# Optimization experiments

Measured on AMD Instinct MI355X. Metric: run time of the kernel, lower is better.

The kernel has to match this reference:

```python
import jax, jax.numpy as jnp
import numpy as np

TAU = 0.95
COEF = 0.5
LOG_CLAMP = -100.0  # torch BCELoss clamps log terms at -100


def setup_inputs() -> dict:
    key = jax.random.key(0)
    k1, k2, k3, k4, k5 = jax.random.split(key, 5)
    B, L = 4096, 2048
    eps = 1e-4
    # probabilities in (eps, 1-eps) so log / log1p are finite
    def prob(k, shape):
        return jax.random.uniform(k, shape, dtype=jnp.float32, minval=eps, maxval=1.0 - eps)
    truncation_output = prob(k1, (B, L, 1))
    view_1_output = prob(k2, (B, L, 1))
    view_2_output = prob(k3, (B, L, 1))
    view_3_output = prob(k4, (B, L, 1))
    labels = (jax.random.uniform(k5, (B, L)) < 0.1).astype(jnp.float32)
    return {
        "truncation_output": truncation_output,
        "view_1_output": view_1_output,
        "view_2_output": view_2_output,
        "view_3_output": view_3_output,
        "labels": labels,
    }


def _bce_div_batch(p, y):
    # nn.BCELoss() (mean reduction) then .div(batch_size)
    logp = jnp.maximum(jnp.log(p), LOG_CLAMP)
    log1mp = jnp.maximum(jnp.log1p(-p), LOG_CLAMP)
    bce = -jnp.mean(y * logp + (1.0 - y) * log1mp)
    return bce / p.shape[0]


def _f1_matrix(labels):
    # r[i, j] = F1(labels[i], cutoff=j+1), vectorized via cumsum
    B, L = labels.shape
    cum = jnp.cumsum(labels, axis=1)                       # rel@(j+1)
    k = jnp.arange(1, L + 1, dtype=labels.dtype)           # cutoff
    total = cum[:, -1:]                                    # total relevant per row
    # P = cum/k, R = cum/total -> F1 = 2*cum/(k+total); 0 when no hits
    return jnp.where(cum > 0, 2.0 * cum / (k + total), 0.0)


def reference(truncation_output, view_1_output, view_2_output, view_3_output, labels):
    B = truncation_output.shape[0]
    v1 = _bce_div_batch(view_1_output[..., 0], labels)
    v2 = _bce_div_batch(view_2_output[..., 0], labels)
    v3 = _bce_div_batch(view_3_output[..., 0], labels)

    r = _f1_matrix(labels)                                 # [B, L]
    q = jax.nn.softmax(r / TAU, axis=-1)                   # softmax over list dim
    log_out = jnp.log(truncation_output[..., 0] / TAU)
    trunc_loss = -jnp.sum(log_out * q) / B

    return COEF * trunc_loss + (1.0 - COEF) * (v1 + v2 + v3)
```

## Files before the change

kernel.cpp:

```cpp
#include <hip/hip_runtime.h>

#define B_DIM 4096
#define L_DIM 2048
#define TPB   256
#define EPT   8
#define NWAVE (TPB / 64)
#define TAU_INV 1.0526315789473684f

__global__ __launch_bounds__(TPB) void milecut_row_kernel(
    const float* __restrict__ trunc,
    const float* __restrict__ view1,
    const float* __restrict__ view2,
    const float* __restrict__ view3,
    const float* __restrict__ labels,
    float* __restrict__ partials)
{
    const int row  = blockIdx.x;
    const int t    = threadIdx.x;
    const int lane = t & 63;
    const int wave = t >> 6;
    const size_t rowOff = (size_t)row * L_DIM;

    const float4* y4 = (const float4*)(labels + rowOff) + t * 2;
    const float4* t4 = (const float4*)(trunc  + rowOff) + t * 2;
    const float4* p1 = (const float4*)(view1  + rowOff) + t * 2;
    const float4* p2 = (const float4*)(view2  + rowOff) + t * 2;
    const float4* p3 = (const float4*)(view3  + rowOff) + t * 2;
    float4 ya = y4[0], yb = y4[1];
    float4 ta = t4[0], tb = t4[1];
    float4 v1a = p1[0], v1b = p1[1];
    float4 v2a = p2[0], v2b = p2[1];
    float4 v3a = p3[0], v3b = p3[1];

    float y[EPT]  = {ya.x, ya.y, ya.z, ya.w, yb.x, yb.y, yb.z, yb.w};

    float lsum = 0.f;
    #pragma unroll
    for (int k = 0; k < EPT; ++k) lsum += y[k];

    float v = lsum;
    #pragma unroll
    for (int off = 1; off < 64; off <<= 1) {
        float n = __shfl_up(v, off, 64);
        if (lane >= off) v += n;
    }
    float waveTotal = __shfl(v, 63, 64);

    __shared__ float wtot[NWAVE];
    __shared__ float red[NWAVE][3];
    if (lane == 63) wtot[wave] = waveTotal;
    __syncthreads();
    float wavePrefix = 0.f, total = 0.f;
    #pragma unroll
    for (int w = 0; w < NWAVE; ++w) {
        float wt = wtot[w];
        if (w < wave) wavePrefix += wt;
        total += wt;
    }
    float run = wavePrefix + (v - lsum);

    float x[EPT];
    float esum = 0.f;
    #pragma unroll
    for (int k = 0; k < EPT; ++k) {
        run += y[k];
        float denom = (float)(t * EPT + k + 1) + total;
        float r = (run > 0.f) ? (2.f * run) / denom : 0.f;
        x[k] = __expf(r * TAU_INV);
        esum += x[k];
    }

    float tv[EPT] = {ta.x, ta.y, ta.z, ta.w, tb.x, tb.y, tb.z, tb.w};
    float wtr = 0.f;
    #pragma unroll
    for (int k = 0; k < EPT; ++k) wtr += __logf(tv[k] * TAU_INV) * x[k];

    float pv1[EPT] = {v1a.x, v1a.y, v1a.z, v1a.w, v1b.x, v1b.y, v1b.z, v1b.w};
    float pv2[EPT] = {v2a.x, v2a.y, v2a.z, v2a.w, v2b.x, v2b.y, v2b.z, v2b.w};
    float pv3[EPT] = {v3a.x, v3a.y, v3a.z, v3a.w, v3b.x, v3b.y, v3b.z, v3b.w};
    float bce = 0.f;
    #pragma unroll
    for (int k = 0; k < EPT; ++k) {
        bool pos = (y[k] > 0.5f);
        float s1 = pos ? pv1[k] : (1.0f - pv1[k]);
        float s2 = pos ? pv2[k] : (1.0f - pv2[k]);
        float s3 = pos ? pv3[k] : (1.0f - pv3[k]);
        bce += fmaxf(__logf(s1), -100.0f);
        bce += fmaxf(__logf(s2), -100.0f);
        bce += fmaxf(__logf(s3), -100.0f);
    }

    #pragma unroll
    for (int off = 32; off > 0; off >>= 1) {
        esum += __shfl_down(esum, off, 64);
        wtr  += __shfl_down(wtr,  off, 64);
        bce  += __shfl_down(bce,  off, 64);
    }
    if (lane == 0) { red[wave][0] = esum; red[wave][1] = wtr; red[wave][2] = bce; }
    __syncthreads();

    if (t == 0) {
        float es = 0.f, wt = 0.f, bc = 0.f;
        #pragma unroll
        for (int w = 0; w < NWAVE; ++w) {
            es += red[w][0]; wt += red[w][1]; bc += red[w][2];
        }
        partials[row]         = wt / es;
        partials[B_DIM + row] = bc;
    }
}

__global__ __launch_bounds__(TPB) void milecut_final_kernel(
    const float* __restrict__ partials, float* __restrict__ out)
{
    const int t = threadIdx.x;
    float st = 0.f, sb = 0.f;
    for (int i = t; i < B_DIM; i += TPB) {
        st += partials[i];
        sb += partials[B_DIM + i];
    }
    #pragma unroll
    for (int off = 32; off > 0; off >>= 1) {
        st += __shfl_down(st, off, 64);
        sb += __shfl_down(sb, off, 64);
    }
    __shared__ float s1[NWAVE];
    __shared__ float s2[NWAVE];
    const int lane = t & 63, wave = t >> 6;
    if (lane == 0) { s1[wave] = st; s2[wave] = sb; }
    __syncthreads();
    if (t == 0) {
        double St = 0.0, Sb = 0.0;
        #pragma unroll
        for (int w = 0; w < NWAVE; ++w) { St += (double)s1[w]; Sb += (double)s2[w]; }
        double trunc_loss = -St / (double)B_DIM;
        double vsum = -Sb / ((double)B_DIM * (double)L_DIM * (double)B_DIM);
        out[0] = (float)(0.5 * trunc_loss + 0.5 * vsum);
    }
}

extern "C" void kernel_launch(void* const* d_in, const int* in_sizes, int n_in,
                              void* d_out, int out_size, void* d_ws, size_t ws_size,
                              hipStream_t stream) {
    const float* trunc  = (const float*)d_in[0];
    const float* v1     = (const float*)d_in[1];
    const float* v2     = (const float*)d_in[2];
    const float* v3     = (const float*)d_in[3];
    const float* labels = (const float*)d_in[4];

    float* partials = (float*)d_ws;

    milecut_row_kernel<<<B_DIM, TPB, 0, stream>>>(trunc, v1, v2, v3, labels, partials);
    milecut_final_kernel<<<1, TPB, 0, stream>>>(partials, (float*)d_out);
}
```

Before: 181.0 us.

## Map one wavefront per row and prefetch lane-strided float4 groups

Each wavefront now processes a whole row, with 4 rows per block, so block-level shared-memory scans and __syncthreads barriers are gone. Loads are lane-strided float4 groups: all labels are loaded up front, and the other four input streams are software-prefetched one group ahead. The label prefix scan runs per group with wave shuffles, and the division is replaced by a hardware reciprocal approximation. The final reduction reads partials as float4. Per-lane register use rises and precision of the reciprocal is slightly lower.

```diff
diff --git a/kernel.cpp b/kernel.cpp
--- a/kernel.cpp
+++ b/kernel.cpp
@@ -3,8 +3,8 @@
 #define B_DIM 4096
 #define L_DIM 2048
 #define TPB   256
-#define EPT   8
-#define NWAVE (TPB / 64)
+#define RPB   4
+#define NG    8
 #define TAU_INV 1.0526315789473684f
 
 __global__ __launch_bounds__(TPB) void milecut_row_kernel(
@@ -15,79 +15,85 @@
     const float* __restrict__ labels,
     float* __restrict__ partials)
 {
-    const int row  = blockIdx.x;
-    const int t    = threadIdx.x;
-    const int lane = t & 63;
-    const int wave = t >> 6;
+    const int lane = threadIdx.x & 63;
+    const int wave = threadIdx.x >> 6;
+    const int row  = blockIdx.x * RPB + wave;
     const size_t rowOff = (size_t)row * L_DIM;
 
-    const float4* y4 = (const float4*)(labels + rowOff) + t * 2;
-    const float4* t4 = (const float4*)(trunc  + rowOff) + t * 2;
-    const float4* p1 = (const float4*)(view1  + rowOff) + t * 2;
-    const float4* p2 = (const float4*)(view2  + rowOff) + t * 2;
-    const float4* p3 = (const float4*)(view3  + rowOff) + t * 2;
-    float4 ya = y4[0], yb = y4[1];
-    float4 ta = t4[0], tb = t4[1];
-    float4 v1a = p1[0], v1b = p1[1];
-    float4 v2a = p2[0], v2b = p2[1];
-    float4 v3a = p3[0], v3b = p3[1];
+    const float4* yb = (const float4*)(labels + rowOff);
+    float4 yv[NG];
+    #pragma unroll
+    for (int g = 0; g < NG; ++g) yv[g] = yb[g * 64 + lane];
 
-    float y[EPT]  = {ya.x, ya.y, ya.z, ya.w, yb.x, yb.y, yb.z, yb.w};
+    const float4* tb = (const float4*)(trunc + rowOff);
+    const float4* b1 = (const float4*)(view1 + rowOff);
+    const float4* b2 = (const float4*)(view2 + rowOff);
+    const float4* b3 = (const float4*)(view3 + rowOff);
+    float4 tc = tb[lane], c1 = b1[lane], c2 = b2[lane], c3 = b3[lane];
 
-    float lsum = 0.f;
+    float s4[NG];
+    unsigned mask = 0;
     #pragma unroll
-    for (int k = 0; k < EPT; ++k) lsum += y[k];
+    for (int g = 0; g < NG; ++g) {
+        float4 y = yv[g];
+        s4[g] = (y.x + y.y) + (y.z + y.w);
+        unsigned m = (y.x > 0.5f ? 1u : 0u) | (y.y > 0.5f ? 2u : 0u)
+                   | (y.z > 0.5f ? 4u : 0u) | (y.w > 0.5f ? 8u : 0u);
+        mask |= m << (g * 4);
+    }
 
-    float v = lsum;
+    float incl[NG];
+    #pragma unroll
+    for (int g = 0; g < NG; ++g) incl[g] = s4[g];
     #pragma unroll
     for (int off = 1; off < 64; off <<= 1) {
-        float n = __shfl_up(v, off, 64);
-        if (lane >= off) v += n;
+        #pragma unroll
+        for (int g = 0; g < NG; ++g) {
+            float n = __shfl_up(incl[g], off, 64);
+            if (lane >= off) incl[g] += n;
+        }
     }
-    float waveTotal = __shfl(v, 63, 64);
+    float gpre[NG];
+    float G = 0.f;
+    #pragma unroll
+    for (int g = 0; g < NG; ++g) {
+        float gt = __shfl(incl[g], 63, 64);
+        gpre[g] = G;
+        G += gt;
+    }
+    const float total = G;
 
-    __shared__ float wtot[NWAVE];
-    __shared__ float red[NWAVE][3];
-    if (lane == 63) wtot[wave] = waveTotal;
-    __syncthreads();
-    float wavePrefix = 0.f, total = 0.f;
+    float esum = 0.f, wtr = 0.f, bce = 0.f;
+    const float two_tauinv = 2.0f * TAU_INV;
     #pragma unroll
-    for (int w = 0; w < NWAVE; ++w) {
-        float wt = wtot[w];
-        if (w < wave) wavePrefix += wt;
-        total += wt;
-    }
-    float run = wavePrefix + (v - lsum);
-
-    float x[EPT];
-    float esum = 0.f;
-    #pragma unroll
-    for (int k = 0; k < EPT; ++k) {
-        run += y[k];
-        float denom = (float)(t * EPT + k + 1) + total;
-        float r = (run > 0.f) ? (2.f * run) / denom : 0.f;
-        x[k] = __expf(r * TAU_INV);
-        esum += x[k];
-    }
-
-    float tv[EPT] = {ta.x, ta.y, ta.z, ta.w, tb.x, tb.y, tb.z, tb.w};
-    float wtr = 0.f;
-    #pragma unroll
-    for (int k = 0; k < EPT; ++k) wtr += __logf(tv[k] * TAU_INV) * x[k];
-
-    float pv1[EPT] = {v1a.x, v1a.y, v1a.z, v1a.w, v1b.x, v1b.y, v1b.z, v1b.w};
-    float pv2[EPT] = {v2a.x, v2a.y, v2a.z, v2a.w, v2b.x, v2b.y, v2b.z, v2b.w};
-    float pv3[EPT] = {v3a.x, v3a.y, v3a.z, v3a.w, v3b.x, v3b.y, v3b.z, v3b.w};
-    float bce = 0.f;
-    #pragma unroll
-    for (int k = 0; k < EPT; ++k) {
-        bool pos = (y[k] > 0.5f);
-        float s1 = pos ? pv1[k] : (1.0f - pv1[k]);
-        float s2 = pos ? pv2[k] : (1.0f - pv2[k]);
-        float s3 = pos ? pv3[k] : (1.0f - pv3[k]);
-        bce += fmaxf(__logf(s1), -100.0f);
-        bce += fmaxf(__logf(s2), -100.0f);
-        bce += fmaxf(__logf(s3), -100.0f);
+    for (int g = 0; g < NG; ++g) {
+        float tv[4] = {tc.x, tc.y, tc.z, tc.w};
+        float a1[4] = {c1.x, c1.y, c1.z, c1.w};
+        float a2[4] = {c2.x, c2.y, c2.z, c2.w};
+        float a3[4] = {c3.x, c3.y, c3.z, c3.w};
+        if (g + 1 < NG) {
+            tc = tb[(g + 1) * 64 + lane];
+            c1 = b1[(g + 1) * 64 + lane];
+            c2 = b2[(g + 1) * 64 + lane];
+            c3 = b3[(g + 1) * 64 + lane];
+        }
+        float run = gpre[g] + (incl[g] - s4[g]);
+        const float base = (float)(g * 256 + lane * 4 + 1) + total;
+        #pragma unroll
+        for (int j = 0; j < 4; ++j) {
+            bool pos = (mask >> (g * 4 + j)) & 1u;
+            run += pos ? 1.0f : 0.0f;
+            float denom = base + (float)j;
+            float e = __expf((two_tauinv * run) * __builtin_amdgcn_rcpf(denom));
+            esum += e;
+            wtr += __logf(tv[j] * TAU_INV) * e;
+            float q1 = pos ? a1[j] : 1.0f - a1[j];
+            float q2 = pos ? a2[j] : 1.0f - a2[j];
+            float q3 = pos ? a3[j] : 1.0f - a3[j];
+            bce += fmaxf(__logf(q1), -100.0f);
+            bce += fmaxf(__logf(q2), -100.0f);
+            bce += fmaxf(__logf(q3), -100.0f);
+        }
     }
 
     #pragma unroll
@@ -96,17 +102,9 @@
         wtr  += __shfl_down(wtr,  off, 64);
         bce  += __shfl_down(bce,  off, 64);
     }
-    if (lane == 0) { red[wave][0] = esum; red[wave][1] = wtr; red[wave][2] = bce; }
-    __syncthreads();
-
-    if (t == 0) {
-        float es = 0.f, wt = 0.f, bc = 0.f;
-        #pragma unroll
-        for (int w = 0; w < NWAVE; ++w) {
-            es += red[w][0]; wt += red[w][1]; bc += red[w][2];
-        }
-        partials[row]         = wt / es;
-        partials[B_DIM + row] = bc;
+    if (lane == 0) {
+        partials[row]         = wtr / esum;
+        partials[B_DIM + row] = bce;
     }
 }
 
@@ -114,25 +112,31 @@
     const float* __restrict__ partials, float* __restrict__ out)
 {
     const int t = threadIdx.x;
+    const float4* p4 = (const float4*)partials;
     float st = 0.f, sb = 0.f;
-    for (int i = t; i < B_DIM; i += TPB) {
-        st += partials[i];
-        sb += partials[B_DIM + i];
+    #pragma unroll
+    for (int i = 0; i < 4; ++i) {
+        float4 a = p4[t + 256 * i];
+        st += (a.x + a.y) + (a.z + a.w);
+    }
+    #pragma unroll
+    for (int i = 4; i < 8; ++i) {
+        float4 a = p4[t + 256 * i];
+        sb += (a.x + a.y) + (a.z + a.w);
     }
     #pragma unroll
     for (int off = 32; off > 0; off >>= 1) {
         st += __shfl_down(st, off, 64);
         sb += __shfl_down(sb, off, 64);
     }
-    __shared__ float s1[NWAVE];
-    __shared__ float s2[NWAVE];
+    __shared__ float s1[RPB], s2[RPB];
     const int lane = t & 63, wave = t >> 6;
     if (lane == 0) { s1[wave] = st; s2[wave] = sb; }
     __syncthreads();
     if (t == 0) {
         double St = 0.0, Sb = 0.0;
         #pragma unroll
-        for (int w = 0; w < NWAVE; ++w) { St += (double)s1[w]; Sb += (double)s2[w]; }
+        for (int w = 0; w < RPB; ++w) { St += (double)s1[w]; Sb += (double)s2[w]; }
         double trunc_loss = -St / (double)B_DIM;
         double vsum = -Sb / ((double)B_DIM * (double)L_DIM * (double)B_DIM);
         out[0] = (float)(0.5 * trunc_loss + 0.5 * vsum);
@@ -150,6 +154,6 @@
 
     float* partials = (float*)d_ws;
 
-    milecut_row_kernel<<<B_DIM, TPB, 0, stream>>>(trunc, v1, v2, v3, labels, partials);
+    milecut_row_kernel<<<B_DIM / RPB, TPB, 0, stream>>>(trunc, v1, v2, v3, labels, partials);
     milecut_final_kernel<<<1, TPB, 0, stream>>>(partials, (float*)d_out);
 }
```

Result: no change. 183.5 us (+1.4%).

## Process four rows per block with register prefetch and bitmask popcount scan

Applied to the files above, without the earlier changes.

Each block now handles four rows and prefetches the next row's five input vectors into registers while it computes the current row. The label prefix scan packs two popcounts into one 16-bit-split integer and runs a single integer shuffle scan, and divisions become hardware reciprocals. Per-thread element mapping changes to coalesced float4 at t and t+256. The aim is to hide memory latency and trim per-row ALU and sync overhead in a bandwidth-bound kernel, at the cost of more registers and fewer blocks.

```diff
diff --git a/kernel.cpp b/kernel.cpp
--- a/kernel.cpp
+++ b/kernel.cpp
@@ -3,8 +3,9 @@
 #define B_DIM 4096
 #define L_DIM 2048
 #define TPB   256
-#define EPT   8
-#define NWAVE (TPB / 64)
+#define RPB   4
+#define NW    4
+#define NBLK  (B_DIM / RPB)
 #define TAU_INV 1.0526315789473684f
 
 __global__ __launch_bounds__(TPB) void milecut_row_kernel(
@@ -15,98 +16,131 @@
     const float* __restrict__ labels,
     float* __restrict__ partials)
 {
-    const int row  = blockIdx.x;
     const int t    = threadIdx.x;
     const int lane = t & 63;
-    const int wave = t >> 6;
-    const size_t rowOff = (size_t)row * L_DIM;
+    const int wv   = t >> 6;
+    const int row0 = blockIdx.x * RPB;
 
-    const float4* y4 = (const float4*)(labels + rowOff) + t * 2;
-    const float4* t4 = (const float4*)(trunc  + rowOff) + t * 2;
-    const float4* p1 = (const float4*)(view1  + rowOff) + t * 2;
-    const float4* p2 = (const float4*)(view2  + rowOff) + t * 2;
-    const float4* p3 = (const float4*)(view3  + rowOff) + t * 2;
-    float4 ya = y4[0], yb = y4[1];
-    float4 ta = t4[0], tb = t4[1];
-    float4 v1a = p1[0], v1b = p1[1];
-    float4 v2a = p2[0], v2b = p2[1];
-    float4 v3a = p3[0], v3b = p3[1];
+    __shared__ unsigned swtot[NW];
+    __shared__ float    srow[RPB][NW][2];
+    __shared__ float    sbce[NW];
 
-    float y[EPT]  = {ya.x, ya.y, ya.z, ya.w, yb.x, yb.y, yb.z, yb.w};
+    size_t off = (size_t)row0 * L_DIM;
+    float4 nya = ((const float4*)(labels + off))[t];
+    float4 nyb = ((const float4*)(labels + off))[t + 256];
+    float4 nta = ((const float4*)(trunc  + off))[t];
+    float4 ntb = ((const float4*)(trunc  + off))[t + 256];
+    float4 n1a = ((const float4*)(view1  + off))[t];
+    float4 n1b = ((const float4*)(view1  + off))[t + 256];
+    float4 n2a = ((const float4*)(view2  + off))[t];
+    float4 n2b = ((const float4*)(view2  + off))[t + 256];
+    float4 n3a = ((const float4*)(view3  + off))[t];
+    float4 n3b = ((const float4*)(view3  + off))[t + 256];
 
-    float lsum = 0.f;
+    float bce = 0.f;
+
     #pragma unroll
-    for (int k = 0; k < EPT; ++k) lsum += y[k];
+    for (int rr = 0; rr < RPB; ++rr) {
+        float4 ya = nya, yb = nyb, ta = nta, tb = ntb;
+        float4 u1a = n1a, u1b = n1b, u2a = n2a, u2b = n2b, u3a = n3a, u3b = n3b;
+        if (rr + 1 < RPB) {
+            size_t o2 = (size_t)(row0 + rr + 1) * L_DIM;
+            nya = ((const float4*)(labels + o2))[t];
+            nyb = ((const float4*)(labels + o2))[t + 256];
+            nta = ((const float4*)(trunc  + o2))[t];
+            ntb = ((const float4*)(trunc  + o2))[t + 256];
+            n1a = ((const float4*)(view1  + o2))[t];
+            n1b = ((const float4*)(view1  + o2))[t + 256];
+            n2a = ((const float4*)(view2  + o2))[t];
+            n2b = ((const float4*)(view2  + o2))[t + 256];
+            n3a = ((const float4*)(view3  + o2))[t];
+            n3b = ((const float4*)(view3  + o2))[t + 256];
+        }
 
-    float v = lsum;
-    #pragma unroll
-    for (int off = 1; off < 64; off <<= 1) {
-        float n = __shfl_up(v, off, 64);
-        if (lane >= off) v += n;
-    }
-    float waveTotal = __shfl(v, 63, 64);
+        unsigned m1 = (ya.x > 0.5f ? 1u : 0u) | (ya.y > 0.5f ? 2u : 0u)
+                    | (ya.z > 0.5f ? 4u : 0u) | (ya.w > 0.5f ? 8u : 0u);
+        unsigned m2 = (yb.x > 0.5f ? 1u : 0u) | (yb.y > 0.5f ? 2u : 0u)
+                    | (yb.z > 0.5f ? 4u : 0u) | (yb.w > 0.5f ? 8u : 0u);
+        unsigned pv = (unsigned)__popc(m1) | ((unsigned)__popc(m2) << 16);
 
-    __shared__ float wtot[NWAVE];
-    __shared__ float red[NWAVE][3];
-    if (lane == 63) wtot[wave] = waveTotal;
-    __syncthreads();
-    float wavePrefix = 0.f, total = 0.f;
-    #pragma unroll
-    for (int w = 0; w < NWAVE; ++w) {
-        float wt = wtot[w];
-        if (w < wave) wavePrefix += wt;
-        total += wt;
-    }
-    float run = wavePrefix + (v - lsum);
+        unsigned incl = pv;
+        #pragma unroll
+        for (int o = 1; o < 64; o <<= 1) {
+            unsigned n = (unsigned)__shfl_up((int)incl, o, 64);
+            if (lane >= o) incl += n;
+        }
+        if (lane == 63) swtot[wv] = incl;
+        __syncthreads();
+        unsigned pref = 0, tot = 0;
+        #pragma unroll
+        for (int w = 0; w < NW; ++w) {
+            unsigned x = swtot[w];
+            if (w < wv) pref += x;
+            tot += x;
+        }
+        __syncthreads();
 
-    float x[EPT];
-    float esum = 0.f;
-    #pragma unroll
-    for (int k = 0; k < EPT; ++k) {
-        run += y[k];
-        float denom = (float)(t * EPT + k + 1) + total;
-        float r = (run > 0.f) ? (2.f * run) / denom : 0.f;
-        x[k] = __expf(r * TAU_INV);
-        esum += x[k];
-    }
+        unsigned eo    = incl - pv;
+        unsigned excl1 = (pref & 0xffffu) + (eo & 0xffffu);
+        unsigned tot1  = tot & 0xffffu;
+        unsigned excl2 = tot1 + (pref >> 16) + (eo >> 16);
+        float ftotal   = (float)(tot1 + (tot >> 16));
 
-    float tv[EPT] = {ta.x, ta.y, ta.z, ta.w, tb.x, tb.y, tb.z, tb.w};
-    float wtr = 0.f;
-    #pragma unroll
-    for (int k = 0; k < EPT; ++k) wtr += __logf(tv[k] * TAU_INV) * x[k];
+        float esum = 0.f, wtr = 0.f;
+        float tva[4] = {ta.x, ta.y, ta.z, ta.w};
+        float tvb[4] = {tb.x, tb.y, tb.z, tb.w};
+        float w1a[4] = {u1a.x, u1a.y, u1a.z, u1a.w};
+        float w1b[4] = {u1b.x, u1b.y, u1b.z, u1b.w};
+        float w2a[4] = {u2a.x, u2a.y, u2a.z, u2a.w};
+        float w2b[4] = {u2b.x, u2b.y, u2b.z, u2b.w};
+        float w3a[4] = {u3a.x, u3a.y, u3a.z, u3a.w};
+        float w3b[4] = {u3b.x, u3b.y, u3b.z, u3b.w};
+        const float two_tauinv = 2.0f * TAU_INV;
+        #pragma unroll
+        for (int j = 0; j < 4; ++j) {
+            unsigned c1 = excl1 + (unsigned)__popc(m1 & ((2u << j) - 1u));
+            float d1 = (float)(4 * t + j + 1) + ftotal;
+            float e1 = __expf(two_tauinv * (float)c1 * __builtin_amdgcn_rcpf(d1));
+            esum += e1;
+            wtr  += __logf(tva[j] * TAU_INV) * e1;
+            bool p1 = (m1 >> j) & 1u;
+            bce += fmaxf(__logf(p1 ? w1a[j] : 1.f - w1a[j]), -100.f);
+            bce += fmaxf(__logf(p1 ? w2a[j] : 1.f - w2a[j]), -100.f);
+            bce += fmaxf(__logf(p1 ? w3a[j] : 1.f - w3a[j]), -100.f);
+            unsigned c2 = excl2 + (unsigned)__popc(m2 & ((2u << j) - 1u));
+            float d2 = (float)(1024 + 4 * t + j + 1) + ftotal;
+            float e2 = __expf(two_tauinv * (float)c2 * __builtin_amdgcn_rcpf(d2));
+            esum += e2;
+            wtr  += __logf(tvb[j] * TAU_INV) * e2;
+            bool p2 = (m2 >> j) & 1u;
+            bce += fmaxf(__logf(p2 ? w1b[j] : 1.f - w1b[j]), -100.f);
+            bce += fmaxf(__logf(p2 ? w2b[j] : 1.f - w2b[j]), -100.f);
+            bce += fmaxf(__logf(p2 ? w3b[j] : 1.f - w3b[j]), -100.f);
+        }
 
-    float pv1[EPT] = {v1a.x, v1a.y, v1a.z, v1a.w, v1b.x, v1b.y, v1b.z, v1b.w};
-    float pv2[EPT] = {v2a.x, v2a.y, v2a.z, v2a.w, v2b.x, v2b.y, v2b.z, v2b.w};
-    float pv3[EPT] = {v3a.x, v3a.y, v3a.z, v3a.w, v3b.x, v3b.y, v3b.z, v3b.w};
-    float bce = 0.f;
-    #pragma unroll
-    for (int k = 0; k < EPT; ++k) {
-        bool pos = (y[k] > 0.5f);
-        float s1 = pos ? pv1[k] : (1.0f - pv1[k]);
-        float s2 = pos ? pv2[k] : (1.0f - pv2[k]);
-        float s3 = pos ? pv3[k] : (1.0f - pv3[k]);
-        bce += fmaxf(__logf(s1), -100.0f);
-        bce += fmaxf(__logf(s2), -100.0f);
-        bce += fmaxf(__logf(s3), -100.0f);
+        #pragma unroll
+        for (int o = 32; o > 0; o >>= 1) {
+            esum += __shfl_down(esum, o, 64);
+            wtr  += __shfl_down(wtr,  o, 64);
+        }
+        if (lane == 0) { srow[rr][wv][0] = esum; srow[rr][wv][1] = wtr; }
     }
 
     #pragma unroll
-    for (int off = 32; off > 0; off >>= 1) {
-        esum += __shfl_down(esum, off, 64);
-        wtr  += __shfl_down(wtr,  off, 64);
-        bce  += __shfl_down(bce,  off, 64);
-    }
-    if (lane == 0) { red[wave][0] = esum; red[wave][1] = wtr; red[wave][2] = bce; }
+    for (int o = 32; o > 0; o >>= 1) bce += __shfl_down(bce, o, 64);
+    if (lane == 0) sbce[wv] = bce;
     __syncthreads();
-
     if (t == 0) {
-        float es = 0.f, wt = 0.f, bc = 0.f;
+        float btot = sbce[0] + sbce[1] + sbce[2] + sbce[3];
+        float atr = 0.f;
         #pragma unroll
-        for (int w = 0; w < NWAVE; ++w) {
-            es += red[w][0]; wt += red[w][1]; bc += red[w][2];
+        for (int rr = 0; rr < RPB; ++rr) {
+            float es = srow[rr][0][0] + srow[rr][1][0] + srow[rr][2][0] + srow[rr][3][0];
+            float wt = srow[rr][0][1] + srow[rr][1][1] + srow[rr][2][1] + srow[rr][3][1];
+            atr += wt / es;
         }
-        partials[row]         = wt / es;
-        partials[B_DIM + row] = bc;
+        partials[blockIdx.x]        = atr;
+        partials[NBLK + blockIdx.x] = btot;
     }
 }
 
@@ -114,25 +148,24 @@
     const float* __restrict__ partials, float* __restrict__ out)
 {
     const int t = threadIdx.x;
-    float st = 0.f, sb = 0.f;
-    for (int i = t; i < B_DIM; i += TPB) {
-        st += partials[i];
-        sb += partials[B_DIM + i];
+    const float4* p4 = (const float4*)partials;
+    float4 a = p4[t];
+    float4 b = p4[256 + t];
+    float st = (a.x + a.y) + (a.z + a.w);
+    float sb = (b.x + b.y) + (b.z + b.w);
+    #pragma unroll
+    for (int o = 32; o > 0; o >>= 1) {
+        st += __shfl_down(st, o, 64);
+        sb += __shfl_down(sb, o, 64);
     }
-    #pragma unroll
-    for (int off = 32; off > 0; off >>= 1) {
-        st += __shfl_down(st, off, 64);
-        sb += __shfl_down(sb, off, 64);
-    }
-    __shared__ float s1[NWAVE];
-    __shared__ float s2[NWAVE];
-    const int lane = t & 63, wave = t >> 6;
-    if (lane == 0) { s1[wave] = st; s2[wave] = sb; }
+    __shared__ float s1[NW], s2[NW];
+    const int lane = t & 63, wv = t >> 6;
+    if (lane == 0) { s1[wv] = st; s2[wv] = sb; }
     __syncthreads();
     if (t == 0) {
         double St = 0.0, Sb = 0.0;
         #pragma unroll
-        for (int w = 0; w < NWAVE; ++w) { St += (double)s1[w]; Sb += (double)s2[w]; }
+        for (int w = 0; w < NW; ++w) { St += (double)s1[w]; Sb += (double)s2[w]; }
         double trunc_loss = -St / (double)B_DIM;
         double vsum = -Sb / ((double)B_DIM * (double)L_DIM * (double)B_DIM);
         out[0] = (float)(0.5 * trunc_loss + 0.5 * vsum);
@@ -150,6 +183,6 @@
 
     float* partials = (float*)d_ws;
 
-    milecut_row_kernel<<<B_DIM, TPB, 0, stream>>>(trunc, v1, v2, v3, labels, partials);
+    milecut_row_kernel<<<NBLK, TPB, 0, stream>>>(trunc, v1, v2, v3, labels, partials);
     milecut_final_kernel<<<1, TPB, 0, stream>>>(partials, (float*)d_out);
 }
```

Result: no change. 181.2 us (+0.1%).
